# Optimization experiments

Hardware: AMD Instinct MI355X
Metric: run time of the kernel (lower is better)

The kernel has to match this reference:

```python
import jax, jax.numpy as jnp
import numpy as np

B, S, D, H = 512, 100, 2, 256


def _lstm_cell(x, h, c, Wih, Whh, bih, bhh):
    # torch gate order: i, f, g, o
    g = x @ Wih.T + bih + h @ Whh.T + bhh
    i, f, gg, o = jnp.split(g, 4, axis=-1)
    c = jax.nn.sigmoid(f) * c + jax.nn.sigmoid(i) * jnp.tanh(gg)
    h = jax.nn.sigmoid(o) * jnp.tanh(c)
    return h, c


def setup_inputs() -> dict:
    key = jax.random.key(0)
    ks = jax.random.split(key, 18)
    w = lambda k, shape, s=0.1: (jax.random.normal(k, shape, jnp.float32) * s)
    return {
        "x": jax.random.uniform(ks[0], (B, S, D), jnp.float32),
        "enc_Wih": w(ks[1], (4 * H, D)), "enc_Whh": w(ks[2], (4 * H, H)),
        "enc_bih": w(ks[3], (4 * H,)), "enc_bhh": w(ks[4], (4 * H,)),
        "dec_Wih": w(ks[5], (4 * H, D)), "dec_Whh": w(ks[6], (4 * H, H)),
        "dec_bih": w(ks[7], (4 * H,)), "dec_bhh": w(ks[8], (4 * H,)),
        "att_We": w(ks[9], (H, H)), "att_be": w(ks[10], (H,)),
        "att_Wd": w(ks[11], (H, H)), "att_bd": w(ks[12], (H,)),
        "V_w": w(ks[13], (H,)), "V_b": w(ks[14], (1,)),
        "start": jax.random.normal(ks[15], (D,), jnp.float32),
    }


def reference(x, enc_Wih, enc_Whh, enc_bih, enc_bhh,
              dec_Wih, dec_Whh, dec_bih, dec_bhh,
              att_We, att_be, att_Wd, att_bd, V_w, V_b, start):
    b, s, _ = x.shape
    h0 = jnp.zeros((b, H), x.dtype)
    c0 = jnp.zeros((b, H), x.dtype)

    # ---- encoder LSTM over sequence ----
    def enc_step(carry, xt):
        h, c = carry
        h, c = _lstm_cell(xt, h, c, enc_Wih, enc_Whh, enc_bih, enc_bhh)
        return (h, c), h

    (h, c), enc_out = jax.lax.scan(enc_step, (h0, c0), jnp.swapaxes(x, 0, 1))
    enc_out = jnp.swapaxes(enc_out, 0, 1)  # [B,S,H]

    # W_encoder applied once (same values every decode step)
    enc_proj = jnp.einsum('bsh,kh->bsk', enc_out, att_We) + att_be  # [B,S,H]

    # ---- decoder: S greedy pointer steps ----
    mask0 = jnp.zeros((b, s), dtype=bool)
    din0 = jnp.broadcast_to(start, (b, D))

    def dec_step(carry, _):
        h, c, mask, din = carry
        h, c = _lstm_cell(din, h, c, dec_Wih, dec_Whh, dec_bih, dec_bhh)
        dec_proj = h @ att_Wd.T + att_bd                  # [B,H]
        u = jnp.tanh(enc_proj + dec_proj[:, None, :])      # [B,S,H]
        scores = u @ V_w + V_b[0]                          # [B,S]
        scores = jnp.where(mask, -jnp.inf, scores)
        log_probs = jax.nn.log_softmax(scores, axis=1)
        sel = jnp.argmax(log_probs, axis=1)                # [B]
        lp = jnp.take_along_axis(log_probs, sel[:, None], axis=1)[:, 0]
        mask = mask | jax.nn.one_hot(sel, s, dtype=bool)
        din = jnp.take_along_axis(x, sel[:, None, None], axis=1)[:, 0, :]
        return (h, c, mask, din), (sel, lp)

    (h, c, mask, din), (tour_t, lp_t) = jax.lax.scan(
        dec_step, (h, c, mask0, din0), None, length=s)

    tour = jnp.swapaxes(tour_t, 0, 1)            # [B,S]
    log_probability = jnp.sum(lp_t, axis=0)       # [B]
    return tour, log_probability, h
```

## Files before the change

### kernel.cpp

```cpp
#include <hip/hip_runtime.h>


#define B_WHE  0ull
#define B_WHD  (B_WHE + 1048576ull)
#define B_WET  (B_WHD + 1048576ull)
#define B_WDT  (B_WET + 262144ull)
#define B_WXE  (B_WDT + 262144ull)
#define B_WXD  (B_WXE + 32768ull)
#define B_EP   (B_WXD + 32768ull)

__device__ __forceinline__ double sigmoid_d(double x) {
  return 1.0 / (1.0 + exp(-x));
}

__device__ __forceinline__ double exp_pos_d(double a) {
  const double L2E    = 1.4426950408889634074;
  const double LN2_HI = 6.9314718036912381649e-01;
  const double LN2_LO = 1.9082149292705877000e-10;
  const double nf = rint(a * L2E);
  double t = __builtin_fma(-nf, LN2_HI, a);
  t = __builtin_fma(-nf, LN2_LO, t);
  double p = 2.0876756987868099e-09;
  p = __builtin_fma(p, t, 2.5052108385441720e-08);
  p = __builtin_fma(p, t, 2.7557319223985888e-07);
  p = __builtin_fma(p, t, 2.7557319223985893e-06);
  p = __builtin_fma(p, t, 2.4801587301587302e-05);
  p = __builtin_fma(p, t, 1.9841269841269841e-04);
  p = __builtin_fma(p, t, 1.3888888888888889e-03);
  p = __builtin_fma(p, t, 8.3333333333333332e-03);
  p = __builtin_fma(p, t, 4.1666666666666664e-02);
  p = __builtin_fma(p, t, 1.6666666666666666e-01);
  p = __builtin_fma(p, t, 5.0e-01);
  p = __builtin_fma(p, t, 1.0);
  p = __builtin_fma(p, t, 1.0);
  return ldexp(p, (int)nf);
}

__device__ __forceinline__ double fast_div_d(double a, double b) {
  double r = __builtin_amdgcn_rcp(b);
  r = __builtin_fma(__builtin_fma(-b, r, 1.0), r, r);
  r = __builtin_fma(__builtin_fma(-b, r, 1.0), r, r);
  double q = a * r;
  q = __builtin_fma(__builtin_fma(-b, q, a), r, q);
  return q;
}

__device__ __forceinline__ double tanh_att_d(double x) {
  const double ax = fmin(fabs(x), 22.0);
  const double e  = exp_pos_d(2.0 * ax);
  const double r  = 1.0 - fast_div_d(2.0, e + 1.0);
  return copysign(r, x);
}

__device__ __forceinline__ double shfl_xor_d(double v, int m) {
  const long long l = __double_as_longlong(v);
  int lo = (int)(l & 0xffffffffll), hi = (int)(l >> 32);
  lo = __shfl_xor(lo, m, 64);
  hi = __shfl_xor(hi, m, 64);
  return __longlong_as_double(((long long)hi << 32) | (unsigned int)lo);
}

__device__ __forceinline__ double wave64_sum_d(double v) {
  #pragma unroll
  for (int m = 1; m < 64; m <<= 1) v += shfl_xor_d(v, m);
  return v;
}

struct SMem {
  double sredf[104];
  unsigned char slist[104];
  float  evals[104];
  float  bc_lp;
  int    bc_sel;
};

extern "C" __global__ void ptrnet_prep(
    const float* __restrict__ eWih, const float* __restrict__ eWhh,
    const float* __restrict__ ebih, const float* __restrict__ ebhh,
    const float* __restrict__ dWih, const float* __restrict__ dWhh,
    const float* __restrict__ dbih, const float* __restrict__ dbhh,
    const float* __restrict__ We,  const float* __restrict__ Wd,
    char* __restrict__ wsb)
{
  const int idx = blockIdx.x * blockDim.x + threadIdx.x;
  const int stride = gridDim.x * blockDim.x;
  float* WHE = (float*)(wsb + B_WHE);
  float* WHD = (float*)(wsb + B_WHD);
  float* WET = (float*)(wsb + B_WET);
  float* WDT = (float*)(wsb + B_WDT);
  double* WXE = (double*)(wsb + B_WXE);
  double* WXD = (double*)(wsb + B_WXD);

  for (int i = idx; i < 256*256*4; i += stride) {
    const int g = i & 3, u = (i >> 2) & 255, k = i >> 10;
    WHE[i] = eWhh[(g*256 + u)*256 + k];
    WHD[i] = dWhh[(g*256 + u)*256 + k];
  }
  for (int i = idx; i < 256*256; i += stride) {
    const int u = i & 255, k = i >> 8;
    WET[i] = We[u*256 + k];
    WDT[i] = Wd[u*256 + k];
  }
  for (int i = idx; i < 256*16; i += stride) {
    const int f = i & 15, u = i >> 4;
    double ve = 0.0, vd = 0.0;
    if (f < 8) {
      const int gg = f >> 1, d = f & 1;
      ve = (double)eWih[(gg*256+u)*2 + d];
      vd = (double)dWih[(gg*256+u)*2 + d];
    } else if (f < 12) {
      const int gg = f - 8;
      ve = (double)ebih[gg*256+u] + (double)ebhh[gg*256+u];
      vd = (double)dbih[gg*256+u] + (double)dbhh[gg*256+u];
    }
    WXE[i] = ve;
    WXD[i] = vd;
  }
}

extern "C" __global__ void __launch_bounds__(1024, 4)
ptrnet_main(char* __restrict__ wsb,
            const float* __restrict__ x,
            const float* __restrict__ be,
            const float* __restrict__ bd,
            const float* __restrict__ Vw,
            const float* __restrict__ Vb,
            const float* __restrict__ start,
            float* __restrict__ out)
{
  __shared__ double hls[2][2][256];
  __shared__ double dls[2][256];
  __shared__ double pred[2][3][256][5];
  __shared__ SMem sm[2];
  const int b0   = blockIdx.x * 2;
  const int b1   = b0 + 1;
  const int tid  = threadIdx.x;
  const int u    = tid & 255;
  const int q    = tid >> 8;
  const int k0   = q << 6;
  const int lane = tid & 63;
  const int w = __builtin_amdgcn_readfirstlane(tid >> 6);

  const float* WHE = (const float*)(wsb + B_WHE);
  const float* WHD = (const float*)(wsb + B_WHD);
  const float* WET = (const float*)(wsb + B_WET);
  const float* WDT = (const float*)(wsb + B_WDT);
  const double* wxE = (const double*)(wsb + B_WXE) + u*16;
  const double* wxD = (const double*)(wsb + B_WXD) + u*16;
  double* ep0 = (double*)(wsb + B_EP) + (size_t)b0*25600;
  double* ep1 = (double*)(wsb + B_EP) + (size_t)b1*25600;

  const double be_u = (double)be[u];
  const double bd_u = (double)bd[u];
  const double vb0  = (double)Vb[0];
  const double vq0 = (double)Vw[lane*4 + 0];
  const double vq1 = (double)Vw[lane*4 + 1];
  const double vq2 = (double)Vw[lane*4 + 2];
  const double vq3 = (double)Vw[lane*4 + 3];

  double c_state = 0.0;
  int par = 0;
  if (tid < 256) { hls[0][0][tid] = 0.0; hls[0][1][tid] = 0.0; }
  __syncthreads();

  for (int t = 0; t < 100; ++t) {
    const double x00 = (double)x[(b0*100 + t)*2 + 0];
    const double x01 = (double)x[(b0*100 + t)*2 + 1];
    const double x10 = (double)x[(b1*100 + t)*2 + 0];
    const double x11 = (double)x[(b1*100 + t)*2 + 1];
    double p0 = 0.0, p1 = 0.0, p2 = 0.0, p3 = 0.0, p4 = 0.0;
    double q0 = 0.0, q1 = 0.0, q2 = 0.0, q3 = 0.0, q4 = 0.0;
    const double* h0 = hls[par][0];
    const double* h1 = hls[par][1];
    #pragma unroll 8
    for (int k = k0; k < k0 + 64; ++k) {
      const double hk0 = h0[k];
      const double hk1 = h1[k];
      const float4 wf = *(const float4*)(WHE + k*1024 + u*4);
      const float  we = WET[k*256 + u];
      const double wx = (double)wf.x, wy = (double)wf.y;
      const double wz = (double)wf.z, ww = (double)wf.w;
      const double wv = (double)we;
      p0 = fma(wx, hk0, p0);  q0 = fma(wx, hk1, q0);
      p1 = fma(wy, hk0, p1);  q1 = fma(wy, hk1, q1);
      p2 = fma(wz, hk0, p2);  q2 = fma(wz, hk1, q2);
      p3 = fma(ww, hk0, p3);  q3 = fma(ww, hk1, q3);
      p4 = fma(wv, hk0, p4);  q4 = fma(wv, hk1, q4);
    }
    if (q == 0) {
      pred[1][0][u][0] = q0; pred[1][0][u][1] = q1; pred[1][0][u][2] = q2;
      pred[1][0][u][3] = q3; pred[1][0][u][4] = q4;
    } else if (q == 1) {
      pred[0][0][u][0] = p0; pred[0][0][u][1] = p1; pred[0][0][u][2] = p2;
      pred[0][0][u][3] = p3; pred[0][0][u][4] = p4;
    } else {
      const int sl = q - 1;
      pred[0][sl][u][0] = p0; pred[0][sl][u][1] = p1; pred[0][sl][u][2] = p2;
      pred[0][sl][u][3] = p3; pred[0][sl][u][4] = p4;
      pred[1][sl][u][0] = q0; pred[1][sl][u][1] = q1; pred[1][sl][u][2] = q2;
      pred[1][sl][u][3] = q3; pred[1][sl][u][4] = q4;
    }
    __syncthreads();
    if (q < 2) {
      const double o0 = q ? q0 : p0, o1 = q ? q1 : p1, o2 = q ? q2 : p2;
      const double o3 = q ? q3 : p3, o4 = q ? q4 : p4;
      const double a0 = o0 + pred[q][0][u][0] + pred[q][1][u][0] + pred[q][2][u][0];
      const double a1 = o1 + pred[q][0][u][1] + pred[q][1][u][1] + pred[q][2][u][1];
      const double a2 = o2 + pred[q][0][u][2] + pred[q][1][u][2] + pred[q][2][u][2];
      const double a3 = o3 + pred[q][0][u][3] + pred[q][1][u][3] + pred[q][2][u][3];
      const double ae = o4 + pred[q][0][u][4] + pred[q][1][u][4] + pred[q][2][u][4];
      const double xg0 = q ? x10 : x00;
      const double xg1 = q ? x11 : x01;
      const double gi = a0 + fma(wxE[0], xg0, fma(wxE[1], xg1, wxE[8]));
      const double gf = a1 + fma(wxE[2], xg0, fma(wxE[3], xg1, wxE[9]));
      const double gg = a2 + fma(wxE[4], xg0, fma(wxE[5], xg1, wxE[10]));
      const double go = a3 + fma(wxE[6], xg0, fma(wxE[7], xg1, wxE[11]));
      const double cn = sigmoid_d(gf)*c_state + sigmoid_d(gi)*tanh(gg);
      const double hn = sigmoid_d(go)*tanh(cn);
      c_state = cn;
      if (t > 0) (q ? ep1 : ep0)[(t-1)*256 + u] = ae + be_u;
      hls[par ^ 1][q][u] = hn;
    }
    __syncthreads();
    par ^= 1;
  }
  {
    double ae0 = 0.0, ae1 = 0.0;
    const double* h0 = hls[par][0];
    const double* h1 = hls[par][1];
    #pragma unroll 8
    for (int k = k0; k < k0 + 64; ++k) {
      const double wv = (double)WET[k*256 + u];
      ae0 = fma(wv, h0[k], ae0);
      ae1 = fma(wv, h1[k], ae1);
    }
    if (q == 0) {
      pred[1][0][u][0] = ae1;
    } else if (q == 1) {
      pred[0][0][u][0] = ae0;
    } else {
      const int sl = q - 1;
      pred[0][sl][u][0] = ae0;
      pred[1][sl][u][0] = ae1;
    }
    __syncthreads();
    if (q < 2) {
      const double own = q ? ae1 : ae0;
      const double ae = own + pred[q][0][u][0] + pred[q][1][u][0] + pred[q][2][u][0];
      (q ? ep1 : ep0)[99*256 + u] = ae + be_u;
    }
    __syncthreads();
  }

  unsigned long long ma0 = 0ull, ma1 = 0ull;
  unsigned long long mb0 = 0ull, mb1 = 0ull;
  float lp_acc = 0.0f;

  {
    const double sx0 = (double)start[0];
    const double sx1 = (double)start[1];
    double p0 = 0.0, p1 = 0.0, p2 = 0.0, p3 = 0.0;
    double q0 = 0.0, q1 = 0.0, q2 = 0.0, q3 = 0.0;
    const double* h0 = hls[par][0];
    const double* h1 = hls[par][1];
    #pragma unroll 8
    for (int k = k0; k < k0 + 64; ++k) {
      const double hk0 = h0[k];
      const double hk1 = h1[k];
      const float4 wf = *(const float4*)(WHD + k*1024 + u*4);
      const double wx = (double)wf.x, wy = (double)wf.y;
      const double wz = (double)wf.z, ww = (double)wf.w;
      p0 = fma(wx, hk0, p0);  q0 = fma(wx, hk1, q0);
      p1 = fma(wy, hk0, p1);  q1 = fma(wy, hk1, q1);
      p2 = fma(wz, hk0, p2);  q2 = fma(wz, hk1, q2);
      p3 = fma(ww, hk0, p3);  q3 = fma(ww, hk1, q3);
    }
    if (q == 0) {
      pred[1][0][u][0] = q0; pred[1][0][u][1] = q1;
      pred[1][0][u][2] = q2; pred[1][0][u][3] = q3;
    } else if (q == 1) {
      pred[0][0][u][0] = p0; pred[0][0][u][1] = p1;
      pred[0][0][u][2] = p2; pred[0][0][u][3] = p3;
    } else {
      const int sl = q - 1;
      pred[0][sl][u][0] = p0; pred[0][sl][u][1] = p1;
      pred[0][sl][u][2] = p2; pred[0][sl][u][3] = p3;
      pred[1][sl][u][0] = q0; pred[1][sl][u][1] = q1;
      pred[1][sl][u][2] = q2; pred[1][sl][u][3] = q3;
    }
    __syncthreads();
    if (q < 2) {
      const double o0 = q ? q0 : p0, o1 = q ? q1 : p1;
      const double o2 = q ? q2 : p2, o3 = q ? q3 : p3;
      const double a0 = o0 + pred[q][0][u][0] + pred[q][1][u][0] + pred[q][2][u][0];
      const double a1 = o1 + pred[q][0][u][1] + pred[q][1][u][1] + pred[q][2][u][1];
      const double a2 = o2 + pred[q][0][u][2] + pred[q][1][u][2] + pred[q][2][u][2];
      const double a3 = o3 + pred[q][0][u][3] + pred[q][1][u][3] + pred[q][2][u][3];
      const double gi = a0 + fma(wxD[0], sx0, fma(wxD[1], sx1, wxD[8]));
      const double gf = a1 + fma(wxD[2], sx0, fma(wxD[3], sx1, wxD[9]));
      const double gg = a2 + fma(wxD[4], sx0, fma(wxD[5], sx1, wxD[10]));
      const double go = a3 + fma(wxD[6], sx0, fma(wxD[7], sx1, wxD[11]));
      const double cn = sigmoid_d(gf)*c_state + sigmoid_d(gi)*tanh(gg);
      const double hn = sigmoid_d(go)*tanh(cn);
      c_state = cn;
      hls[par ^ 1][q][u] = hn;
    }
    __syncthreads();
    par ^= 1;
  }

  for (int t = 0; t < 100; ++t) {
    double go0, go1, go2, go3, dpo;
    {
      double p0 = 0.0, p1 = 0.0, p2 = 0.0, p3 = 0.0, pd = 0.0;
      double q0 = 0.0, q1 = 0.0, q2 = 0.0, q3 = 0.0, qd = 0.0;
      const double* h0 = hls[par][0];
      const double* h1 = hls[par][1];
      #pragma unroll 8
      for (int k = k0; k < k0 + 64; ++k) {
        const double hk0 = h0[k];
        const double hk1 = h1[k];
        const float4 wf = *(const float4*)(WHD + k*1024 + u*4);
        const float  wd = WDT[k*256 + u];
        const double wx = (double)wf.x, wy = (double)wf.y;
        const double wz = (double)wf.z, ww = (double)wf.w;
        const double wv = (double)wd;
        p0 = fma(wx, hk0, p0);  q0 = fma(wx, hk1, q0);
        p1 = fma(wy, hk0, p1);  q1 = fma(wy, hk1, q1);
        p2 = fma(wz, hk0, p2);  q2 = fma(wz, hk1, q2);
        p3 = fma(ww, hk0, p3);  q3 = fma(ww, hk1, q3);
        pd = fma(wv, hk0, pd);  qd = fma(wv, hk1, qd);
      }
      if (q == 0) {
        pred[1][0][u][0] = q0; pred[1][0][u][1] = q1; pred[1][0][u][2] = q2;
        pred[1][0][u][3] = q3; pred[1][0][u][4] = qd;
      } else if (q == 1) {
        pred[0][0][u][0] = p0; pred[0][0][u][1] = p1; pred[0][0][u][2] = p2;
        pred[0][0][u][3] = p3; pred[0][0][u][4] = pd;
      } else {
        const int sl = q - 1;
        pred[0][sl][u][0] = p0; pred[0][sl][u][1] = p1; pred[0][sl][u][2] = p2;
        pred[0][sl][u][3] = p3; pred[0][sl][u][4] = pd;
        pred[1][sl][u][0] = q0; pred[1][sl][u][1] = q1; pred[1][sl][u][2] = q2;
        pred[1][sl][u][3] = q3; pred[1][sl][u][4] = qd;
      }
      go0 = q ? q0 : p0;  go1 = q ? q1 : p1;
      go2 = q ? q2 : p2;  go3 = q ? q3 : p3;
      dpo = q ? qd : pd;
    }
    __syncthreads();
    if (q < 2) {
      dls[q][u] = dpo + pred[q][0][u][4] + pred[q][1][u][4] + pred[q][2][u][4]
                  + bd_u;
      const unsigned long long km0 = q ? mb0 : ma0;
      const unsigned long long km1 = q ? mb1 : ma1;
      const unsigned long long um0 = ~km0;
      const unsigned long long um1 = (~km1) & 0xFFFFFFFFFull;
      if (u < 100) {
        bool unm; int pre;
        if (u < 64) {
          unm = ((um0 >> u) & 1ull) != 0ull;
          pre = __popcll(um0 & ((1ull << u) - 1ull));
        } else {
          const int r = u - 64;
          unm = ((um1 >> r) & 1ull) != 0ull;
          pre = __popcll(um0) + __popcll(um1 & ((1ull << r) - 1ull));
        }
        if (unm) sm[q].slist[pre] = (unsigned char)u;
      }
    }
    __syncthreads();
    {
      const int scnt = 100 - t;
      const int bw = w >> 3;
      const int wi = w & 7;
      const double* epb = bw ? ep1 : ep0;
      const double dpq0 = dls[bw][lane*4 + 0];
      const double dpq1 = dls[bw][lane*4 + 1];
      const double dpq2 = dls[bw][lane*4 + 2];
      const double dpq3 = dls[bw][lane*4 + 3];
      int i = wi;
      int scur = 0;
      double2 c01, c23;
      if (i < scnt) {
        scur = (int)sm[bw].slist[i];
        const double* er = epb + scur*256 + lane*4;
        c01 = *(const double2*)(er);
        c23 = *(const double2*)(er + 2);
      }
      while (i < scnt) {
        const int inext = i + 8;
        int snext = 0;
        double2 n01 = c01, n23 = c23;
        if (inext < scnt) {
          snext = (int)sm[bw].slist[inext];
          const double* er = epb + snext*256 + lane*4;
          n01 = *(const double2*)(er);
          n23 = *(const double2*)(er + 2);
        }
        double p =        tanh_att_d(c01.x + dpq0) * vq0;
        p = __builtin_fma(tanh_att_d(c01.y + dpq1), vq1, p);
        p = __builtin_fma(tanh_att_d(c23.x + dpq2), vq2, p);
        p = __builtin_fma(tanh_att_d(c23.y + dpq3), vq3, p);
        p = wave64_sum_d(p);
        if (lane == 0) sm[bw].sredf[scur] = p;
        scur = snext; c01 = n01; c23 = n23; i = inext;
      }
    }
    __syncthreads();
    if ((w & 7) == 0) {
      const int bb = w >> 3;
      const unsigned long long km0 = bb ? mb0 : ma0;
      const unsigned long long km1 = bb ? mb1 : ma1;
      const bool mk0 = ((km0 >> lane) & 1ull) != 0ull;
      const bool mk1 = (lane < 36) ? (((km1 >> lane) & 1ull) != 0ull) : true;
      const int  s1i = 64 + (lane < 36 ? lane : 0);
      const float sc0 = mk0 ? -__builtin_inff()
                            : (float)(sm[bb].sredf[lane] + vb0);
      const float sc1 = mk1 ? -__builtin_inff()
                            : (float)(sm[bb].sredf[s1i] + vb0);
      float mv = fmaxf(sc0, sc1);
      #pragma unroll
      for (int mm = 1; mm < 64; mm <<= 1)
        mv = fmaxf(mv, __shfl_xor(mv, mm, 64));
      sm[bb].evals[lane] = expf(__fsub_rn(sc0, mv));
      if (lane < 36) sm[bb].evals[64 + lane] = expf(__fsub_rn(sc1, mv));
      asm volatile("s_waitcnt lgkmcnt(0)" ::: "memory");
      __builtin_amdgcn_sched_barrier(0);
      float rr[8];
      #pragma unroll
      for (int j = 0; j < 8; ++j) rr[j] = sm[bb].evals[j];
      for (int i = 8; i < 96; i += 8) {
        #pragma unroll
        for (int j = 0; j < 8; ++j) rr[j] = __fadd_rn(rr[j], sm[bb].evals[i + j]);
      }
      float res = __fadd_rn(
          __fadd_rn(__fadd_rn(rr[0], rr[1]), __fadd_rn(rr[2], rr[3])),
          __fadd_rn(__fadd_rn(rr[4], rr[5]), __fadd_rn(rr[6], rr[7])));
      res = __fadd_rn(res, sm[bb].evals[96]);
      res = __fadd_rn(res, sm[bb].evals[97]);
      res = __fadd_rn(res, sm[bb].evals[98]);
      res = __fadd_rn(res, sm[bb].evals[99]);
      const float L = logf(res);
      const float lp0 = __fsub_rn(__fsub_rn(sc0, mv), L);
      const float lp1 = (lane < 36)
          ? __fsub_rn(__fsub_rn(sc1, mv), L)
          : -__builtin_inff();
      float bv; int bi;
      if (lp0 >= lp1) { bv = lp0; bi = lane; } else { bv = lp1; bi = 64 + lane; }
      #pragma unroll
      for (int mm = 1; mm < 64; mm <<= 1) {
        const float ov = __shfl_xor(bv, mm, 64);
        const int   oi = __shfl_xor(bi, mm, 64);
        if (ov > bv || (ov == bv && oi < bi)) { bv = ov; bi = oi; }
      }
      if (lane == 0) { sm[bb].bc_sel = bi; sm[bb].bc_lp = bv; }
    }
    __syncthreads();
    const int sel0 = __builtin_amdgcn_readfirstlane(sm[0].bc_sel);
    const int sel1 = __builtin_amdgcn_readfirstlane(sm[1].bc_sel);
    lp_acc = __fadd_rn(lp_acc, sm[q & 1].bc_lp);
    if (sel0 < 64) ma0 |= (1ull << sel0); else ma1 |= (1ull << (sel0 - 64));
    if (sel1 < 64) mb0 |= (1ull << sel1); else mb1 |= (1ull << (sel1 - 64));
    if (tid == 0)   out[b0*100 + t] = (float)sel0;
    if (tid == 256) out[b1*100 + t] = (float)sel1;
    if (t < 99) {
      if (q < 2) {
        const int sel = q ? sel1 : sel0;
        const int bb  = q ? b1 : b0;
        const double xd0 = (double)x[(bb*100 + sel)*2 + 0];
        const double xd1 = (double)x[(bb*100 + sel)*2 + 1];
        const double a0 = go0 + pred[q][0][u][0] + pred[q][1][u][0] + pred[q][2][u][0];
        const double a1 = go1 + pred[q][0][u][1] + pred[q][1][u][1] + pred[q][2][u][1];
        const double a2 = go2 + pred[q][0][u][2] + pred[q][1][u][2] + pred[q][2][u][2];
        const double a3 = go3 + pred[q][0][u][3] + pred[q][1][u][3] + pred[q][2][u][3];
        const double gi = a0 + fma(wxD[0], xd0, fma(wxD[1], xd1, wxD[8]));
        const double gf = a1 + fma(wxD[2], xd0, fma(wxD[3], xd1, wxD[9]));
        const double gg = a2 + fma(wxD[4], xd0, fma(wxD[5], xd1, wxD[10]));
        const double go = a3 + fma(wxD[6], xd0, fma(wxD[7], xd1, wxD[11]));
        const double cn = sigmoid_d(gf)*c_state + sigmoid_d(gi)*tanh(gg);
        const double hn = sigmoid_d(go)*tanh(cn);
        c_state = cn;
        hls[par ^ 1][q][u] = hn;
      }
      par ^= 1;
    }
    __syncthreads();
  }

  if (tid == 0)   out[51200 + b0] = lp_acc;
  if (tid == 256) out[51200 + b1] = lp_acc;
  if (q < 2) out[51712 + (q ? b1 : b0)*256 + u] = (float)hls[par][q][u];
}

extern "C" void kernel_launch(void* const* d_in, const int* in_sizes, int n_in,
                              void* d_out, int out_size, void* d_ws, size_t ws_size,
                              hipStream_t stream) {
  const float* x     = (const float*)d_in[0];
  const float* eWih  = (const float*)d_in[1];
  const float* eWhh  = (const float*)d_in[2];
  const float* ebih  = (const float*)d_in[3];
  const float* ebhh  = (const float*)d_in[4];
  const float* dWih  = (const float*)d_in[5];
  const float* dWhh  = (const float*)d_in[6];
  const float* dbih  = (const float*)d_in[7];
  const float* dbhh  = (const float*)d_in[8];
  const float* We    = (const float*)d_in[9];
  const float* be    = (const float*)d_in[10];
  const float* Wd    = (const float*)d_in[11];
  const float* bd    = (const float*)d_in[12];
  const float* vw    = (const float*)d_in[13];
  const float* vb    = (const float*)d_in[14];
  const float* start = (const float*)d_in[15];
  char* ws    = (char*)d_ws;
  float* outp = (float*)d_out;

  ptrnet_prep<<<dim3(512), dim3(256), 0, stream>>>(
      eWih, eWhh, ebih, ebhh, dWih, dWhh, dbih, dbhh, We, Wd, ws);

  ptrnet_main<<<dim3(256), dim3(1024), 0, stream>>>(ws, x, be, bd, vw, vb,
                                                    start, outp);
}
```

Baseline: 5.897 ms.

## Overlap decoder LSTM gate matvec with attention scoring across wave groups

Each decode step now first computes only the decoder attention projection (W_d·h) across all four thread quarters. After that, half the waves compute attention scores while the other half compute the next step's LSTM gate matvec (W_hh·h), split over two K-halves. This removes one block barrier per step and lets the large gate matvec run concurrently with the tanh-heavy scoring loop. The cost is that attention scoring now runs on 8 waves instead of 16. The shared-memory buffers are merged into one pool, and the softmax waves are reassigned to match the new split.

```diff
diff --git a/kernel.cpp b/kernel.cpp
--- a/kernel.cpp
+++ b/kernel.cpp
@@ -118,6 +118,10 @@
   }
 }
 
+#define PENC(b,sl,uu,st)  pool[((((b)*3 + (sl))*256 + (uu))*5) + (st)]
+#define PDP(b,sl,uu)      pool[(((b)*4 + (sl))*256) + (uu)]
+#define PLSTM(b,g,uu,hf)  pool[2048 + ((((b)*4 + (g))*256 + (uu))*2) + (hf)]
+
 extern "C" __global__ void __launch_bounds__(1024, 4)
 ptrnet_main(char* __restrict__ wsb,
             const float* __restrict__ x,
@@ -129,8 +133,7 @@
             float* __restrict__ out)
 {
   __shared__ double hls[2][2][256];
-  __shared__ double dls[2][256];
-  __shared__ double pred[2][3][256][5];
+  __shared__ double pool[7680];
   __shared__ SMem sm[2];
   const int b0   = blockIdx.x * 2;
   const int b1   = b0 + 1;
@@ -157,6 +160,10 @@
   const double vq1 = (double)Vw[lane*4 + 1];
   const double vq2 = (double)Vw[lane*4 + 2];
   const double vq3 = (double)Vw[lane*4 + 3];
+  const double bdq0 = (double)bd[lane*4 + 0];
+  const double bdq1 = (double)bd[lane*4 + 1];
+  const double bdq2 = (double)bd[lane*4 + 2];
+  const double bdq3 = (double)bd[lane*4 + 3];
 
   double c_state = 0.0;
   int par = 0;
@@ -188,27 +195,27 @@
       p4 = fma(wv, hk0, p4);  q4 = fma(wv, hk1, q4);
     }
     if (q == 0) {
-      pred[1][0][u][0] = q0; pred[1][0][u][1] = q1; pred[1][0][u][2] = q2;
-      pred[1][0][u][3] = q3; pred[1][0][u][4] = q4;
+      PENC(1,0,u,0) = q0; PENC(1,0,u,1) = q1; PENC(1,0,u,2) = q2;
+      PENC(1,0,u,3) = q3; PENC(1,0,u,4) = q4;
     } else if (q == 1) {
-      pred[0][0][u][0] = p0; pred[0][0][u][1] = p1; pred[0][0][u][2] = p2;
-      pred[0][0][u][3] = p3; pred[0][0][u][4] = p4;
+      PENC(0,0,u,0) = p0; PENC(0,0,u,1) = p1; PENC(0,0,u,2) = p2;
+      PENC(0,0,u,3) = p3; PENC(0,0,u,4) = p4;
     } else {
       const int sl = q - 1;
-      pred[0][sl][u][0] = p0; pred[0][sl][u][1] = p1; pred[0][sl][u][2] = p2;
-      pred[0][sl][u][3] = p3; pred[0][sl][u][4] = p4;
-      pred[1][sl][u][0] = q0; pred[1][sl][u][1] = q1; pred[1][sl][u][2] = q2;
-      pred[1][sl][u][3] = q3; pred[1][sl][u][4] = q4;
+      PENC(0,sl,u,0) = p0; PENC(0,sl,u,1) = p1; PENC(0,sl,u,2) = p2;
+      PENC(0,sl,u,3) = p3; PENC(0,sl,u,4) = p4;
+      PENC(1,sl,u,0) = q0; PENC(1,sl,u,1) = q1; PENC(1,sl,u,2) = q2;
+      PENC(1,sl,u,3) = q3; PENC(1,sl,u,4) = q4;
     }
     __syncthreads();
     if (q < 2) {
       const double o0 = q ? q0 : p0, o1 = q ? q1 : p1, o2 = q ? q2 : p2;
       const double o3 = q ? q3 : p3, o4 = q ? q4 : p4;
-      const double a0 = o0 + pred[q][0][u][0] + pred[q][1][u][0] + pred[q][2][u][0];
-      const double a1 = o1 + pred[q][0][u][1] + pred[q][1][u][1] + pred[q][2][u][1];
-      const double a2 = o2 + pred[q][0][u][2] + pred[q][1][u][2] + pred[q][2][u][2];
-      const double a3 = o3 + pred[q][0][u][3] + pred[q][1][u][3] + pred[q][2][u][3];
-      const double ae = o4 + pred[q][0][u][4] + pred[q][1][u][4] + pred[q][2][u][4];
+      const double a0 = o0 + PENC(q,0,u,0) + PENC(q,1,u,0) + PENC(q,2,u,0);
+      const double a1 = o1 + PENC(q,0,u,1) + PENC(q,1,u,1) + PENC(q,2,u,1);
+      const double a2 = o2 + PENC(q,0,u,2) + PENC(q,1,u,2) + PENC(q,2,u,2);
+      const double a3 = o3 + PENC(q,0,u,3) + PENC(q,1,u,3) + PENC(q,2,u,3);
+      const double ae = o4 + PENC(q,0,u,4) + PENC(q,1,u,4) + PENC(q,2,u,4);
       const double xg0 = q ? x10 : x00;
       const double xg1 = q ? x11 : x01;
       const double gi = a0 + fma(wxE[0], xg0, fma(wxE[1], xg1, wxE[8]));
@@ -235,18 +242,18 @@
       ae1 = fma(wv, h1[k], ae1);
     }
     if (q == 0) {
-      pred[1][0][u][0] = ae1;
+      PENC(1,0,u,0) = ae1;
     } else if (q == 1) {
-      pred[0][0][u][0] = ae0;
+      PENC(0,0,u,0) = ae0;
     } else {
       const int sl = q - 1;
-      pred[0][sl][u][0] = ae0;
-      pred[1][sl][u][0] = ae1;
+      PENC(0,sl,u,0) = ae0;
+      PENC(1,sl,u,0) = ae1;
     }
     __syncthreads();
     if (q < 2) {
       const double own = q ? ae1 : ae0;
-      const double ae = own + pred[q][0][u][0] + pred[q][1][u][0] + pred[q][2][u][0];
+      const double ae = own + PENC(q,0,u,0) + PENC(q,1,u,0) + PENC(q,2,u,0);
       (q ? ep1 : ep0)[99*256 + u] = ae + be_u;
     }
     __syncthreads();
@@ -276,26 +283,26 @@
       p3 = fma(ww, hk0, p3);  q3 = fma(ww, hk1, q3);
     }
     if (q == 0) {
-      pred[1][0][u][0] = q0; pred[1][0][u][1] = q1;
-      pred[1][0][u][2] = q2; pred[1][0][u][3] = q3;
+      PENC(1,0,u,0) = q0; PENC(1,0,u,1) = q1;
+      PENC(1,0,u,2) = q2; PENC(1,0,u,3) = q3;
     } else if (q == 1) {
-      pred[0][0][u][0] = p0; pred[0][0][u][1] = p1;
-      pred[0][0][u][2] = p2; pred[0][0][u][3] = p3;
+      PENC(0,0,u,0) = p0; PENC(0,0,u,1) = p1;
+      PENC(0,0,u,2) = p2; PENC(0,0,u,3) = p3;
     } else {
       const int sl = q - 1;
-      pred[0][sl][u][0] = p0; pred[0][sl][u][1] = p1;
-      pred[0][sl][u][2] = p2; pred[0][sl][u][3] = p3;
-      pred[1][sl][u][0] = q0; pred[1][sl][u][1] = q1;
-      pred[1][sl][u][2] = q2; pred[1][sl][u][3] = q3;
+      PENC(0,sl,u,0) = p0; PENC(0,sl,u,1) = p1;
+      PENC(0,sl,u,2) = p2; PENC(0,sl,u,3) = p3;
+      PENC(1,sl,u,0) = q0; PENC(1,sl,u,1) = q1;
+      PENC(1,sl,u,2) = q2; PENC(1,sl,u,3) = q3;
     }
     __syncthreads();
     if (q < 2) {
       const double o0 = q ? q0 : p0, o1 = q ? q1 : p1;
       const double o2 = q ? q2 : p2, o3 = q ? q3 : p3;
-      const double a0 = o0 + pred[q][0][u][0] + pred[q][1][u][0] + pred[q][2][u][0];
-      const double a1 = o1 + pred[q][0][u][1] + pred[q][1][u][1] + pred[q][2][u][1];
-      const double a2 = o2 + pred[q][0][u][2] + pred[q][1][u][2] + pred[q][2][u][2];
-      const double a3 = o3 + pred[q][0][u][3] + pred[q][1][u][3] + pred[q][2][u][3];
+      const double a0 = o0 + PENC(q,0,u,0) + PENC(q,1,u,0) + PENC(q,2,u,0);
+      const double a1 = o1 + PENC(q,0,u,1) + PENC(q,1,u,1) + PENC(q,2,u,1);
+      const double a2 = o2 + PENC(q,0,u,2) + PENC(q,1,u,2) + PENC(q,2,u,2);
+      const double a3 = o3 + PENC(q,0,u,3) + PENC(q,1,u,3) + PENC(q,2,u,3);
       const double gi = a0 + fma(wxD[0], sx0, fma(wxD[1], sx1, wxD[8]));
       const double gf = a1 + fma(wxD[2], sx0, fma(wxD[3], sx1, wxD[9]));
       const double gg = a2 + fma(wxD[4], sx0, fma(wxD[5], sx1, wxD[10]));
@@ -310,53 +317,23 @@
   }
 
   for (int t = 0; t < 100; ++t) {
-    double go0, go1, go2, go3, dpo;
     {
-      double p0 = 0.0, p1 = 0.0, p2 = 0.0, p3 = 0.0, pd = 0.0;
-      double q0 = 0.0, q1 = 0.0, q2 = 0.0, q3 = 0.0, qd = 0.0;
+      double pd = 0.0, qd = 0.0;
       const double* h0 = hls[par][0];
       const double* h1 = hls[par][1];
       #pragma unroll 8
       for (int k = k0; k < k0 + 64; ++k) {
-        const double hk0 = h0[k];
-        const double hk1 = h1[k];
-        const float4 wf = *(const float4*)(WHD + k*1024 + u*4);
-        const float  wd = WDT[k*256 + u];
-        const double wx = (double)wf.x, wy = (double)wf.y;
-        const double wz = (double)wf.z, ww = (double)wf.w;
-        const double wv = (double)wd;
-        p0 = fma(wx, hk0, p0);  q0 = fma(wx, hk1, q0);
-        p1 = fma(wy, hk0, p1);  q1 = fma(wy, hk1, q1);
-        p2 = fma(wz, hk0, p2);  q2 = fma(wz, hk1, q2);
-        p3 = fma(ww, hk0, p3);  q3 = fma(ww, hk1, q3);
-        pd = fma(wv, hk0, pd);  qd = fma(wv, hk1, qd);
-      }
-      if (q == 0) {
-        pred[1][0][u][0] = q0; pred[1][0][u][1] = q1; pred[1][0][u][2] = q2;
-        pred[1][0][u][3] = q3; pred[1][0][u][4] = qd;
-      } else if (q == 1) {
-        pred[0][0][u][0] = p0; pred[0][0][u][1] = p1; pred[0][0][u][2] = p2;
-        pred[0][0][u][3] = p3; pred[0][0][u][4] = pd;
-      } else {
-        const int sl = q - 1;
-        pred[0][sl][u][0] = p0; pred[0][sl][u][1] = p1; pred[0][sl][u][2] = p2;
-        pred[0][sl][u][3] = p3; pred[0][sl][u][4] = pd;
-        pred[1][sl][u][0] = q0; pred[1][sl][u][1] = q1; pred[1][sl][u][2] = q2;
-        pred[1][sl][u][3] = q3; pred[1][sl][u][4] = qd;
-      }
-      go0 = q ? q0 : p0;  go1 = q ? q1 : p1;
-      go2 = q ? q2 : p2;  go3 = q ? q3 : p3;
-      dpo = q ? qd : pd;
-    }
-    __syncthreads();
-    if (q < 2) {
-      dls[q][u] = dpo + pred[q][0][u][4] + pred[q][1][u][4] + pred[q][2][u][4]
-                  + bd_u;
-      const unsigned long long km0 = q ? mb0 : ma0;
-      const unsigned long long km1 = q ? mb1 : ma1;
-      const unsigned long long um0 = ~km0;
-      const unsigned long long um1 = (~km1) & 0xFFFFFFFFFull;
-      if (u < 100) {
+        const double wv = (double)WDT[k*256 + u];
+        pd = fma(wv, h0[k], pd);
+        qd = fma(wv, h1[k], qd);
+      }
+      PDP(0,q,u) = pd;
+      PDP(1,q,u) = qd;
+      if (q < 2 && u < 100) {
+        const unsigned long long km0 = q ? mb0 : ma0;
+        const unsigned long long km1 = q ? mb1 : ma1;
+        const unsigned long long um0 = ~km0;
+        const unsigned long long um1 = (~km1) & 0xFFFFFFFFFull;
         bool unm; int pre;
         if (u < 64) {
           unm = ((um0 >> u) & 1ull) != 0ull;
@@ -370,15 +347,19 @@
       }
     }
     __syncthreads();
-    {
+    if (q < 2) {
+      const int bw = q;
+      const int wi = w & 3;
+      const double* epb = bw ? ep1 : ep0;
+      const double dpq0 = PDP(bw,0,lane*4+0) + PDP(bw,1,lane*4+0)
+                        + PDP(bw,2,lane*4+0) + PDP(bw,3,lane*4+0) + bdq0;
+      const double dpq1 = PDP(bw,0,lane*4+1) + PDP(bw,1,lane*4+1)
+                        + PDP(bw,2,lane*4+1) + PDP(bw,3,lane*4+1) + bdq1;
+      const double dpq2 = PDP(bw,0,lane*4+2) + PDP(bw,1,lane*4+2)
+                        + PDP(bw,2,lane*4+2) + PDP(bw,3,lane*4+2) + bdq2;
+      const double dpq3 = PDP(bw,0,lane*4+3) + PDP(bw,1,lane*4+3)
+                        + PDP(bw,2,lane*4+3) + PDP(bw,3,lane*4+3) + bdq3;
       const int scnt = 100 - t;
-      const int bw = w >> 3;
-      const int wi = w & 7;
-      const double* epb = bw ? ep1 : ep0;
-      const double dpq0 = dls[bw][lane*4 + 0];
-      const double dpq1 = dls[bw][lane*4 + 1];
-      const double dpq2 = dls[bw][lane*4 + 2];
-      const double dpq3 = dls[bw][lane*4 + 3];
       int i = wi;
       int scur = 0;
       double2 c01, c23;
@@ -389,7 +370,7 @@
         c23 = *(const double2*)(er + 2);
       }
       while (i < scnt) {
-        const int inext = i + 8;
+        const int inext = i + 4;
         int snext = 0;
         double2 n01 = c01, n23 = c23;
         if (inext < scnt) {
@@ -406,10 +387,33 @@
         if (lane == 0) sm[bw].sredf[scur] = p;
         scur = snext; c01 = n01; c23 = n23; i = inext;
       }
-    }
-    __syncthreads();
-    if ((w & 7) == 0) {
-      const int bb = w >> 3;
+    } else if (t < 99) {
+      const int half = q - 2;
+      const int kk0 = half << 7;
+      double p0 = 0.0, p1 = 0.0, p2 = 0.0, p3 = 0.0;
+      double q0 = 0.0, q1 = 0.0, q2 = 0.0, q3 = 0.0;
+      const double* h0 = hls[par][0];
+      const double* h1 = hls[par][1];
+      #pragma unroll 8
+      for (int k = kk0; k < kk0 + 128; ++k) {
+        const double hk0 = h0[k];
+        const double hk1 = h1[k];
+        const float4 wf = *(const float4*)(WHD + k*1024 + u*4);
+        const double wx = (double)wf.x, wy = (double)wf.y;
+        const double wz = (double)wf.z, ww = (double)wf.w;
+        p0 = fma(wx, hk0, p0);  q0 = fma(wx, hk1, q0);
+        p1 = fma(wy, hk0, p1);  q1 = fma(wy, hk1, q1);
+        p2 = fma(wz, hk0, p2);  q2 = fma(wz, hk1, q2);
+        p3 = fma(ww, hk0, p3);  q3 = fma(ww, hk1, q3);
+      }
+      PLSTM(0,0,u,half) = p0; PLSTM(0,1,u,half) = p1;
+      PLSTM(0,2,u,half) = p2; PLSTM(0,3,u,half) = p3;
+      PLSTM(1,0,u,half) = q0; PLSTM(1,1,u,half) = q1;
+      PLSTM(1,2,u,half) = q2; PLSTM(1,3,u,half) = q3;
+    }
+    __syncthreads();
+    if (w == 0 || w == 5) {
+      const int bb = (w == 5);
       const unsigned long long km0 = bb ? mb0 : ma0;
       const unsigned long long km1 = bb ? mb1 : ma1;
       const bool mk0 = ((km0 >> lane) & 1ull) != 0ull;
@@ -470,10 +474,10 @@
         const int bb  = q ? b1 : b0;
         const double xd0 = (double)x[(bb*100 + sel)*2 + 0];
         const double xd1 = (double)x[(bb*100 + sel)*2 + 1];
-        const double a0 = go0 + pred[q][0][u][0] + pred[q][1][u][0] + pred[q][2][u][0];
-        const double a1 = go1 + pred[q][0][u][1] + pred[q][1][u][1] + pred[q][2][u][1];
-        const double a2 = go2 + pred[q][0][u][2] + pred[q][1][u][2] + pred[q][2][u][2];
-        const double a3 = go3 + pred[q][0][u][3] + pred[q][1][u][3] + pred[q][2][u][3];
+        const double a0 = PLSTM(q,0,u,0) + PLSTM(q,0,u,1);
+        const double a1 = PLSTM(q,1,u,0) + PLSTM(q,1,u,1);
+        const double a2 = PLSTM(q,2,u,0) + PLSTM(q,2,u,1);
+        const double a3 = PLSTM(q,3,u,0) + PLSTM(q,3,u,1);
         const double gi = a0 + fma(wxD[0], xd0, fma(wxD[1], xd1, wxD[8]));
         const double gf = a1 + fma(wxD[2], xd0, fma(wxD[3], xd1, wxD[9]));
         const double gg = a2 + fma(wxD[4], xd0, fma(wxD[5], xd1, wxD[10]));
```

Result: slower. 6.999 ms (+18.7%).
